# Kernel tuning notes

Hardware: AMD Instinct MI355X
Metric: run time of the kernel (lower is better)

Reference implementation:

```python
import jax, jax.numpy as jnp
import numpy as np

B, N, IN_DIM = 2, 2048, 512
D_MODEL, N_HEADS, N_CLASSES = 1024, 16, 1024


def sin_pos_encoding(n, d):
    # Matches SinPositionalEncoding buffer pe[:n]
    pos = jnp.arange(n, dtype=jnp.float32)[:, None]
    div = jnp.exp(jnp.arange(0, d, 2, dtype=jnp.float32) * (-np.log(10000.0) / d))
    pe = jnp.zeros((n, d), dtype=jnp.float32)
    pe = pe.at[:, 0::2].set(jnp.sin(pos * div))
    pe = pe.at[:, 1::2].set(jnp.cos(pos * div))
    return pe


def setup_inputs() -> dict:
    key = jax.random.key(0)
    ks = jax.random.split(key, 9)
    s_emb = (2.0 / (IN_DIM + D_MODEL)) ** 0.5
    s_qk = (2.0 / (2 * D_MODEL)) ** 0.5
    s_v = (2.0 / (D_MODEL + 1)) ** 0.5
    s_o = (2.0 / (N_HEADS + D_MODEL)) ** 0.5
    s_dec = (2.0 / (D_MODEL + N_CLASSES)) ** 0.5
    return {
        'X': jax.random.normal(ks[0], (B, N, IN_DIM), dtype=jnp.float32),
        'emb_w': jax.random.normal(ks[1], (IN_DIM, D_MODEL), dtype=jnp.float32) * s_emb,
        'emb_b': jax.random.normal(ks[2], (D_MODEL,), dtype=jnp.float32) * 0.01,
        'Wq': jax.random.normal(ks[3], (N_HEADS, D_MODEL, D_MODEL), dtype=jnp.float32) * s_qk,
        'Wk': jax.random.normal(ks[4], (N_HEADS, D_MODEL, D_MODEL), dtype=jnp.float32) * s_qk,
        'Wv': jax.random.normal(ks[5], (N_HEADS, D_MODEL, 1), dtype=jnp.float32) * s_v,
        'Wo': jax.random.normal(ks[6], (N_HEADS, D_MODEL), dtype=jnp.float32) * s_o,
        'dec_w': jax.random.normal(ks[7], (D_MODEL, N_CLASSES), dtype=jnp.float32) * s_dec,
        'dec_b': jax.random.normal(ks[8], (N_CLASSES,), dtype=jnp.float32) * 0.01,
    }


def reference(X, emb_w, emb_b, Wq, Wk, Wv, Wo, dec_w, dec_b):
    b, n, _ = X.shape
    d = emb_w.shape[1]
    h = X @ emb_w + emb_b                       # [b, n, d]
    h = h + sin_pos_encoding(n, d)[None]        # positional encoding
    Q = jnp.einsum('bnd,hde->bhne', h, Wq)      # [b, H, n, d]
    K = jnp.einsum('bnd,hde->bhne', h, Wk)      # [b, H, n, d]
    V = jnp.einsum('bnd,hdv->bhnv', h, Wv)      # [b, H, n, 1]
    scores = jnp.einsum('bhqe,bhke->bhqk', Q, K) / jnp.sqrt(jnp.float32(d))
    # mask[:, 0] = 1 is applied MULTIPLICATIVELY before softmax: column 0 -> 0
    scores = scores.at[..., 0].set(0.0)
    attn = jax.nn.softmax(scores, axis=-1)      # [b, H, n, n]
    ctx = jnp.einsum('bhqk,bhkv->bhqv', attn, V)  # [b, H, n, 1]
    ctx = jnp.transpose(ctx, (0, 2, 1, 3)).reshape(b, n, -1)  # [b, n, H]
    out = ctx @ Wo                              # [b, n, d]
    out = out @ dec_w + dec_b                   # [b, n, n_classes]
    return out
```

## Files before the change

kernel.cpp:

```cpp
#include <hip/hip_runtime.h>
#include <cstdint>

typedef __attribute__((ext_vector_type(8))) short bf16x8;
typedef __attribute__((ext_vector_type(4))) float f32x4;

#define B_ 2
#define N_ 2048
#define IN_DIM_ 512
#define D_ 1024
#define H_ 16

__device__ __forceinline__ unsigned short f2bf(float f) {
  uint32_t u = __float_as_uint(f);
  u = u + 0x7fffu + ((u >> 16) & 1u);
  return (unsigned short)(u >> 16);
}
__device__ __forceinline__ float bf2f(unsigned short b) {
  return __uint_as_float(((uint32_t)b) << 16);
}

__device__ __forceinline__ void gll16(const void* g, void* l) {
  __builtin_amdgcn_global_load_lds(
      (const __attribute__((address_space(1))) uint32_t*)g,
      (__attribute__((address_space(3))) uint32_t*)l, 16, 0, 0);
}

__global__ __launch_bounds__(256) void cast_bf16(const float* __restrict__ X,
                                                 unsigned short* __restrict__ O, int n) {
  int i = (blockIdx.x * 256 + threadIdx.x) * 4;
  if (i + 3 < n) {
    f32x4 v = *(const f32x4*)(X + i);
    uint32_t p0 = (uint32_t)f2bf(v[0]) | ((uint32_t)f2bf(v[1]) << 16);
    uint32_t p1 = (uint32_t)f2bf(v[2]) | ((uint32_t)f2bf(v[3]) << 16);
    *(uint32_t*)(O + i) = p0;
    *(uint32_t*)(O + i + 2) = p1;
  }
}

__global__ __launch_bounds__(256) void transpose_cast(const float* __restrict__ W,
                                                      unsigned short* __restrict__ WT,
                                                      int K, int N) {
  __shared__ float t[32][33];
  const int tx = threadIdx.x, ty = threadIdx.y;
  const int x = blockIdx.x * 32 + tx;
  const int y = blockIdx.y * 32 + ty;
  #pragma unroll
  for (int i = 0; i < 4; ++i)
    t[ty + i * 8][tx] = W[(size_t)(y + i * 8) * N + x];
  __syncthreads();
  const int ox = blockIdx.y * 32 + tx;
  #pragma unroll
  for (int i = 0; i < 4; ++i) {
    const int oy = blockIdx.x * 32 + ty + i * 8;
    WT[(size_t)oy * K + ox] = f2bf(t[tx][ty + i * 8]);
  }
}

__global__ __launch_bounds__(256) void gemm_embed(
    const unsigned short* __restrict__ Xbf, const unsigned short* __restrict__ EbT,
    const float* __restrict__ emb_b, unsigned short* __restrict__ Hbf) {
  const int tid = threadIdx.x, l = tid & 63, w = tid >> 6;
  const int wm = w >> 1, wn = w & 1;
  const int bm = blockIdx.y * 128, bn = blockIdx.x * 128;
  __shared__ unsigned short As[128 * 32], Bs[128 * 32];
  const unsigned short* Ab = Xbf + (size_t)bm * IN_DIM_;
  const unsigned short* Bb = EbT + (size_t)bn * IN_DIM_;
  f32x4 acc[4][4] = {};
  const int lr = l >> 2, lc = (l & 3) * 8;
  for (int k0 = 0; k0 < IN_DIM_; k0 += 32) {
    #pragma unroll
    for (int i = 0; i < 2; ++i) {
      const int c = w * 2 + i;
      gll16(Ab + (size_t)(c * 16 + lr) * IN_DIM_ + k0 + lc, As + c * 512);
      gll16(Bb + (size_t)(c * 16 + lr) * IN_DIM_ + k0 + lc, Bs + c * 512);
    }
    __syncthreads();
    bf16x8 af[4], bfr[4];
    #pragma unroll
    for (int f = 0; f < 4; ++f) {
      af[f]  = *(const bf16x8*)(As + (wm * 64 + f * 16 + (l & 15)) * 32 + (l >> 4) * 8);
      bfr[f] = *(const bf16x8*)(Bs + (wn * 64 + f * 16 + (l & 15)) * 32 + (l >> 4) * 8);
    }
    #pragma unroll
    for (int fr = 0; fr < 4; ++fr)
      #pragma unroll
      for (int fc = 0; fc < 4; ++fc)
        acc[fr][fc] = __builtin_amdgcn_mfma_f32_16x16x32_bf16(af[fr], bfr[fc], acc[fr][fc], 0, 0, 0);
    __syncthreads();
  }
  const float kF = -0.017988946039015983f;
  #pragma unroll
  for (int fr = 0; fr < 4; ++fr) {
    #pragma unroll
    for (int fc = 0; fc < 4; ++fc) {
      const int col = bn + wn * 64 + fc * 16 + (l & 15);
      const float eb = emb_b[col];
      const float fac = expf((float)(col >> 1) * kF);
      #pragma unroll
      for (int j = 0; j < 4; ++j) {
        const int row = bm + wm * 64 + fr * 16 + (l >> 4) * 4 + j;
        const float pos = (float)(row & (N_ - 1));
        const float ang = pos * fac;
        const float pe = (col & 1) ? cosf(ang) : sinf(ang);
        float v = acc[fr][fc][j] + eb + pe;
        float o = __shfl_xor(v, 1);
        unsigned short mb = f2bf(v), ob = f2bf(o);
        uint32_t pk = (l & 1) ? ((uint32_t)ob | ((uint32_t)mb << 16))
                              : ((uint32_t)mb | ((uint32_t)ob << 16));
        const bool mine = (l & 1) ? (j >= 2) : (j < 2);
        if (mine)
          *(uint32_t*)(Hbf + (size_t)row * D_ + (col & ~1)) = pk;
      }
    }
  }
}

__global__ __launch_bounds__(256) void gemm_nt(
    const unsigned short* __restrict__ A, const unsigned short* __restrict__ Bm,
    unsigned short* __restrict__ O, int K, long aZ, long bZ, long oZ, int swz) {
  int bx = blockIdx.x, by = blockIdx.y, bz = blockIdx.z;
  if (swz) {
    const int nx = gridDim.x, ny = gridDim.y;
    const int nwg = nx * ny * gridDim.z;
    const int bid = bx + nx * (by + ny * bz);
    const int wid = (bid & 7) * (nwg >> 3) + (bid >> 3);
    bx = wid % nx;
    const int rest = wid / nx;
    by = rest % ny;
    bz = rest / ny;
  }
  const int z = bz;
  const int tid = threadIdx.x, l = tid & 63, w = tid >> 6;
  const int wm = w >> 1, wn = w & 1;
  const int bm = by * 128, bn = bx * 128;
  const int ldo = gridDim.x * 128;
  __shared__ unsigned short As[128 * 32], Bs[128 * 32];
  const unsigned short* Ab = A + (size_t)z * aZ + (size_t)bm * K;
  const unsigned short* Bb = Bm + (size_t)z * bZ + (size_t)bn * K;
  f32x4 acc[4][4] = {};
  const int lr = l >> 2, lc = (l & 3) * 8;
  for (int k0 = 0; k0 < K; k0 += 32) {
    #pragma unroll
    for (int i = 0; i < 2; ++i) {
      const int c = w * 2 + i;
      gll16(Ab + (size_t)(c * 16 + lr) * K + k0 + lc, As + c * 512);
      gll16(Bb + (size_t)(c * 16 + lr) * K + k0 + lc, Bs + c * 512);
    }
    __syncthreads();
    bf16x8 af[4], bfr[4];
    #pragma unroll
    for (int f = 0; f < 4; ++f) {
      af[f]  = *(const bf16x8*)(As + (wm * 64 + f * 16 + (l & 15)) * 32 + (l >> 4) * 8);
      bfr[f] = *(const bf16x8*)(Bs + (wn * 64 + f * 16 + (l & 15)) * 32 + (l >> 4) * 8);
    }
    #pragma unroll
    for (int fr = 0; fr < 4; ++fr)
      #pragma unroll
      for (int fc = 0; fc < 4; ++fc)
        acc[fr][fc] = __builtin_amdgcn_mfma_f32_16x16x32_bf16(af[fr], bfr[fc], acc[fr][fc], 0, 0, 0);
    __syncthreads();
  }
  unsigned short* obase = O + (size_t)z * oZ;
  #pragma unroll
  for (int fr = 0; fr < 4; ++fr) {
    #pragma unroll
    for (int fc = 0; fc < 4; ++fc) {
      const int col = bn + wn * 64 + fc * 16 + (l & 15);
      #pragma unroll
      for (int j = 0; j < 4; ++j) {
        const int row = bm + wm * 64 + fr * 16 + (l >> 4) * 4 + j;
        float v = acc[fr][fc][j];
        float o = __shfl_xor(v, 1);
        unsigned short mb = f2bf(v), ob = f2bf(o);
        uint32_t pk = (l & 1) ? ((uint32_t)ob | ((uint32_t)mb << 16))
                              : ((uint32_t)mb | ((uint32_t)ob << 16));
        const bool mine = (l & 1) ? (j >= 2) : (j < 2);
        if (mine)
          *(uint32_t*)(obase + (size_t)row * ldo + (col & ~1)) = pk;
      }
    }
  }
}

__global__ __launch_bounds__(256) void v_kernel(
    const unsigned short* __restrict__ Hbf, const float* __restrict__ Wv,
    float* __restrict__ V) {
  const int l = threadIdx.x & 63, w = threadIdx.x >> 6;
  const int ng = blockIdx.x * 4 + w;
  const int b = ng >> 11, n = ng & (N_ - 1);
  const unsigned short* hr = Hbf + (size_t)ng * D_;
  float hv[16];
  #pragma unroll
  for (int i = 0; i < 2; ++i) {
    bf16x8 x = *(const bf16x8*)(hr + l * 16 + i * 8);
    #pragma unroll
    for (int j = 0; j < 8; ++j) hv[i * 8 + j] = bf2f((unsigned short)x[j]);
  }
  for (int h = 0; h < H_; ++h) {
    const float* wr = Wv + (size_t)h * D_ + l * 16;
    float s = 0.f;
    #pragma unroll
    for (int i = 0; i < 4; ++i) {
      f32x4 w4 = *(const f32x4*)(wr + i * 4);
      s += hv[i*4+0]*w4[0] + hv[i*4+1]*w4[1] + hv[i*4+2]*w4[2] + hv[i*4+3]*w4[3];
    }
    #pragma unroll
    for (int m = 1; m < 64; m <<= 1) s += __shfl_xor(s, m);
    if (l == 0) V[((size_t)b * H_ + h) * N_ + n] = s;
  }
}

__global__ __launch_bounds__(256) void score_flash(
    const unsigned short* __restrict__ G, const unsigned short* __restrict__ Hb,
    const float* __restrict__ V, float* __restrict__ Pp) {
  const int bid = blockIdx.x;
  const int wid = (bid & 7) * 512 + (bid >> 3);
  const int kt = wid & 15, qt = (wid >> 4) & 15, h = wid >> 8;
  const int tid = threadIdx.x, l = tid & 63, w = tid >> 6;
  const int wm = w >> 1, wn = w & 1;
  __shared__ unsigned short As[2 * 128 * 32], Bs[2 * 128 * 32];
  __shared__ float sb[2][128][2];
  const unsigned short* Ab = G + ((size_t)h * N_ + qt * 128) * D_;
  const unsigned short* Bb = Hb + (size_t)(kt * 128) * D_;
  const float* Vf = V + (size_t)h * N_;
  f32x4 acc[4][4] = {};
  const int lr = l >> 2, lc = (l & 3) * 8;
  for (int k0 = 0; k0 < D_; k0 += 64) {
    #pragma unroll
    for (int half = 0; half < 2; ++half) {
      #pragma unroll
      for (int i = 0; i < 2; ++i) {
        const int c = w * 2 + i;
        gll16(Ab + (size_t)(c * 16 + lr) * D_ + k0 + half * 32 + lc,
              As + half * 4096 + c * 512);
        gll16(Bb + (size_t)(c * 16 + lr) * D_ + k0 + half * 32 + lc,
              Bs + half * 4096 + c * 512);
      }
    }
    __syncthreads();
    #pragma unroll
    for (int half = 0; half < 2; ++half) {
      bf16x8 af[4], bfr[4];
      #pragma unroll
      for (int f = 0; f < 4; ++f) {
        af[f]  = *(const bf16x8*)(As + half * 4096 + (wm * 64 + f * 16 + (l & 15)) * 32 + (l >> 4) * 8);
        bfr[f] = *(const bf16x8*)(Bs + half * 4096 + (wn * 64 + f * 16 + (l & 15)) * 32 + (l >> 4) * 8);
      }
      #pragma unroll
      for (int fr = 0; fr < 4; ++fr)
        #pragma unroll
        for (int fc = 0; fc < 4; ++fc)
          acc[fr][fc] = __builtin_amdgcn_mfma_f32_16x16x32_bf16(af[fr], bfr[fc], acc[fr][fc], 0, 0, 0);
    }
    __syncthreads();
  }
  float vv[4];
  #pragma unroll
  for (int fc = 0; fc < 4; ++fc)
    vv[fc] = Vf[kt * 128 + wn * 64 + fc * 16 + (l & 15)];
  #pragma unroll
  for (int fr = 0; fr < 4; ++fr) {
    #pragma unroll
    for (int j = 0; j < 4; ++j) {
      float s4[4];
      #pragma unroll
      for (int fc = 0; fc < 4; ++fc) s4[fc] = acc[fr][fc][j] * 0.03125f;
      if (kt == 0 && wn == 0 && (l & 15) == 0) s4[0] = 0.0f;
      float ps = 0.f, pv = 0.f;
      #pragma unroll
      for (int fc = 0; fc < 4; ++fc) {
        const float e = __expf(s4[fc] - 8.0f);
        ps += e; pv += e * vv[fc];
      }
      ps += __shfl_xor(ps, 1); pv += __shfl_xor(pv, 1);
      ps += __shfl_xor(ps, 2); pv += __shfl_xor(pv, 2);
      ps += __shfl_xor(ps, 4); pv += __shfl_xor(pv, 4);
      ps += __shfl_xor(ps, 8); pv += __shfl_xor(pv, 8);
      if ((l & 15) == 0) {
        const int r = wm * 64 + fr * 16 + (l >> 4) * 4 + j;
        sb[wn][r][0] = ps; sb[wn][r][1] = pv;
      }
    }
  }
  __syncthreads();
  if (tid < 128) {
    const int r = tid;
    float* p = Pp + (((size_t)h * 16 + kt) * N_ + qt * 128 + r) * 2;
    p[0] = sb[0][r][0] + sb[1][r][0];
    p[1] = sb[0][r][1] + sb[1][r][1];
  }
}

__global__ __launch_bounds__(256) void merge16(const float* __restrict__ Pp,
                                               float* __restrict__ ctx) {
  const int idx = blockIdx.x * 256 + threadIdx.x;
  const int h = idx >> 11, q = idx & (N_ - 1);
  float L = 0.f, O = 0.f;
  #pragma unroll
  for (int kt = 0; kt < 16; ++kt) {
    const float* p = Pp + (((size_t)h * 16 + kt) * N_ + q) * 2;
    L += p[0]; O += p[1];
  }
  ctx[(size_t)q * H_ + h] = O / L;
}

__global__ __launch_bounds__(256) void wodec_kernel(
    const float* __restrict__ Wo, const float* __restrict__ dec_w, float* __restrict__ M) {
  const int idx = blockIdx.x * 256 + threadIdx.x;
  const int h = idx >> 10, c = idx & 1023;
  float s = 0.f;
  #pragma unroll 4
  for (int d = 0; d < D_; ++d) s += Wo[h * D_ + d] * dec_w[(size_t)d * 1024 + c];
  M[idx] = s;
}

__global__ __launch_bounds__(256) void final_kernel(
    const float* __restrict__ ctx, const float* __restrict__ M,
    const float* __restrict__ dec_b, float* __restrict__ out) {
  const int idx = blockIdx.x * 256 + threadIdx.x;
  const int c = idx & 1023;
  const float* cr = ctx + (size_t)(idx >> 10) * H_;
  float s = dec_b[c];
  #pragma unroll
  for (int h = 0; h < H_; ++h) s += cr[h] * M[h * 1024 + c];
  out[idx] = s;
}

extern "C" void kernel_launch(void* const* d_in, const int* in_sizes, int n_in,
                              void* d_out, int out_size, void* d_ws, size_t ws_size,
                              hipStream_t stream) {
  const float* X     = (const float*)d_in[0];
  const float* emb_w = (const float*)d_in[1];
  const float* emb_b = (const float*)d_in[2];
  const float* Wq    = (const float*)d_in[3];
  const float* Wk    = (const float*)d_in[4];
  const float* Wv    = (const float*)d_in[5];
  const float* Wo    = (const float*)d_in[6];
  const float* dec_b = (const float*)d_in[8];
  const float* dec_w = (const float*)d_in[7];
  float* out = (float*)d_out;
  (void)in_sizes; (void)n_in; (void)out_size;

  char* ws = (char*)d_ws;
  unsigned short* Hbf = (unsigned short*)(ws);
  unsigned short* Wkq = (unsigned short*)(ws + ((size_t)8 << 20));
  float* Vb  = (float*)(ws + ((size_t)40 << 20));
  float* ctx = (float*)(ws + ((size_t)40 << 20) + ((size_t)256 << 10));
  float* Mw  = (float*)(ws + ((size_t)40 << 20) + ((size_t)512 << 10));
  char* S = ws + ((size_t)41 << 20);
  unsigned short* Xbf  = (unsigned short*)(S);
  unsigned short* EbT  = (unsigned short*)(S + ((size_t)4 << 20));
  unsigned short* Wqbf = (unsigned short*)(S);
  unsigned short* Wkbf = (unsigned short*)(S + ((size_t)32 << 20));
  unsigned short* G    = (unsigned short*)(S);
  float* Pp = (float*)d_out;

  const size_t need = ((size_t)41 << 20) + ((size_t)64 << 20);
  if (ws_size < need) return;

  cast_bf16<<<2048, 256, 0, stream>>>(X, Xbf, B_ * N_ * IN_DIM_);
  transpose_cast<<<dim3(32, 16, 1), dim3(32, 8), 0, stream>>>(emb_w, EbT, IN_DIM_, D_);
  gemm_embed<<<dim3(8, 32), 256, 0, stream>>>(Xbf, EbT, emb_b, Hbf);
  cast_bf16<<<16384, 256, 0, stream>>>(Wq, Wqbf, H_ * D_ * D_);
  cast_bf16<<<16384, 256, 0, stream>>>(Wk, Wkbf, H_ * D_ * D_);
  gemm_nt<<<dim3(8, 8, 16), 256, 0, stream>>>(Wkbf, Wqbf, Wkq, D_,
                                              (long)D_ * D_, (long)D_ * D_, (long)D_ * D_, 1);
  v_kernel<<<1024, 256, 0, stream>>>(Hbf, Wv, Vb);
  wodec_kernel<<<64, 256, 0, stream>>>(Wo, dec_w, Mw);

  for (int b = 0; b < B_; ++b) {
    const unsigned short* Hb = Hbf + (size_t)b * N_ * D_;
    gemm_nt<<<dim3(8, 16, 16), 256, 0, stream>>>(Hb, Wkq, G, D_,
                                                 0L, (long)D_ * D_, (long)N_ * D_, 1);
    score_flash<<<4096, 256, 0, stream>>>(G, Hb, Vb + (size_t)b * H_ * N_, Pp);
    merge16<<<128, 256, 0, stream>>>(Pp, ctx + (size_t)b * N_ * H_);
  }
  final_kernel<<<16384, 256, 0, stream>>>(ctx, Mw, dec_b, out);
}
```

Before: 874.1 us.

## Merge Wq/Wk casts and V/Wo-dec kernels, deepen gemm_nt K step

Replaces the two separate Wq and Wk bf16 cast launches with one combined launch, and folds the Wo·dec_w product into the V projection kernel as extra blocks. gemm_nt now loads two 32-wide K slices per barrier pair, processing 64 K per iteration. The goal is fewer kernel launches and fewer barriers per K step. The cost is doubled LDS use in gemm_nt, which may lower occupancy.

```diff
diff --git a/kernel.cpp b/kernel.cpp
--- a/kernel.cpp
+++ b/kernel.cpp
@@ -35,6 +35,22 @@
     *(uint32_t*)(O + i) = p0;
     *(uint32_t*)(O + i + 2) = p1;
   }
+}
+
+__global__ __launch_bounds__(256) void cast_bf16x2(const float* __restrict__ X0,
+                                                   const float* __restrict__ X1,
+                                                   unsigned short* __restrict__ O0,
+                                                   unsigned short* __restrict__ O1, int n) {
+  int i = (blockIdx.x * 256 + threadIdx.x) * 4;
+  const bool second = (i >= n);
+  const int j = second ? i - n : i;
+  const float* X = second ? X1 : X0;
+  unsigned short* O = second ? O1 : O0;
+  f32x4 v = *(const f32x4*)(X + j);
+  uint32_t p0 = (uint32_t)f2bf(v[0]) | ((uint32_t)f2bf(v[1]) << 16);
+  uint32_t p1 = (uint32_t)f2bf(v[2]) | ((uint32_t)f2bf(v[3]) << 16);
+  *(uint32_t*)(O + j) = p0;
+  *(uint32_t*)(O + j + 2) = p1;
 }
 
 __global__ __launch_bounds__(256) void transpose_cast(const float* __restrict__ W,
@@ -134,30 +150,38 @@
   const int wm = w >> 1, wn = w & 1;
   const int bm = by * 128, bn = bx * 128;
   const int ldo = gridDim.x * 128;
-  __shared__ unsigned short As[128 * 32], Bs[128 * 32];
+  __shared__ unsigned short As[2 * 128 * 32], Bs[2 * 128 * 32];
   const unsigned short* Ab = A + (size_t)z * aZ + (size_t)bm * K;
   const unsigned short* Bb = Bm + (size_t)z * bZ + (size_t)bn * K;
   f32x4 acc[4][4] = {};
   const int lr = l >> 2, lc = (l & 3) * 8;
-  for (int k0 = 0; k0 < K; k0 += 32) {
-    #pragma unroll
-    for (int i = 0; i < 2; ++i) {
-      const int c = w * 2 + i;
-      gll16(Ab + (size_t)(c * 16 + lr) * K + k0 + lc, As + c * 512);
-      gll16(Bb + (size_t)(c * 16 + lr) * K + k0 + lc, Bs + c * 512);
-    }
-    __syncthreads();
-    bf16x8 af[4], bfr[4];
-    #pragma unroll
-    for (int f = 0; f < 4; ++f) {
-      af[f]  = *(const bf16x8*)(As + (wm * 64 + f * 16 + (l & 15)) * 32 + (l >> 4) * 8);
-      bfr[f] = *(const bf16x8*)(Bs + (wn * 64 + f * 16 + (l & 15)) * 32 + (l >> 4) * 8);
-    }
-    #pragma unroll
-    for (int fr = 0; fr < 4; ++fr)
-      #pragma unroll
-      for (int fc = 0; fc < 4; ++fc)
-        acc[fr][fc] = __builtin_amdgcn_mfma_f32_16x16x32_bf16(af[fr], bfr[fc], acc[fr][fc], 0, 0, 0);
+  for (int k0 = 0; k0 < K; k0 += 64) {
+    #pragma unroll
+    for (int half = 0; half < 2; ++half) {
+      #pragma unroll
+      for (int i = 0; i < 2; ++i) {
+        const int c = w * 2 + i;
+        gll16(Ab + (size_t)(c * 16 + lr) * K + k0 + half * 32 + lc,
+              As + half * 4096 + c * 512);
+        gll16(Bb + (size_t)(c * 16 + lr) * K + k0 + half * 32 + lc,
+              Bs + half * 4096 + c * 512);
+      }
+    }
+    __syncthreads();
+    #pragma unroll
+    for (int half = 0; half < 2; ++half) {
+      bf16x8 af[4], bfr[4];
+      #pragma unroll
+      for (int f = 0; f < 4; ++f) {
+        af[f]  = *(const bf16x8*)(As + half * 4096 + (wm * 64 + f * 16 + (l & 15)) * 32 + (l >> 4) * 8);
+        bfr[f] = *(const bf16x8*)(Bs + half * 4096 + (wn * 64 + f * 16 + (l & 15)) * 32 + (l >> 4) * 8);
+      }
+      #pragma unroll
+      for (int fr = 0; fr < 4; ++fr)
+        #pragma unroll
+        for (int fc = 0; fc < 4; ++fc)
+          acc[fr][fc] = __builtin_amdgcn_mfma_f32_16x16x32_bf16(af[fr], bfr[fc], acc[fr][fc], 0, 0, 0);
+    }
     __syncthreads();
   }
   unsigned short* obase = O + (size_t)z * oZ;
@@ -182,31 +206,41 @@
   }
 }
 
-__global__ __launch_bounds__(256) void v_kernel(
+__global__ __launch_bounds__(256) void v_wodec_kernel(
     const unsigned short* __restrict__ Hbf, const float* __restrict__ Wv,
-    float* __restrict__ V) {
-  const int l = threadIdx.x & 63, w = threadIdx.x >> 6;
-  const int ng = blockIdx.x * 4 + w;
-  const int b = ng >> 11, n = ng & (N_ - 1);
-  const unsigned short* hr = Hbf + (size_t)ng * D_;
-  float hv[16];
-  #pragma unroll
-  for (int i = 0; i < 2; ++i) {
-    bf16x8 x = *(const bf16x8*)(hr + l * 16 + i * 8);
-    #pragma unroll
-    for (int j = 0; j < 8; ++j) hv[i * 8 + j] = bf2f((unsigned short)x[j]);
-  }
-  for (int h = 0; h < H_; ++h) {
-    const float* wr = Wv + (size_t)h * D_ + l * 16;
+    float* __restrict__ V, const float* __restrict__ Wo,
+    const float* __restrict__ dec_w, float* __restrict__ M) {
+  if (blockIdx.x < 1024) {
+    const int l = threadIdx.x & 63, w = threadIdx.x >> 6;
+    const int ng = blockIdx.x * 4 + w;
+    const int b = ng >> 11, n = ng & (N_ - 1);
+    const unsigned short* hr = Hbf + (size_t)ng * D_;
+    float hv[16];
+    #pragma unroll
+    for (int i = 0; i < 2; ++i) {
+      bf16x8 x = *(const bf16x8*)(hr + l * 16 + i * 8);
+      #pragma unroll
+      for (int j = 0; j < 8; ++j) hv[i * 8 + j] = bf2f((unsigned short)x[j]);
+    }
+    for (int h = 0; h < H_; ++h) {
+      const float* wr = Wv + (size_t)h * D_ + l * 16;
+      float s = 0.f;
+      #pragma unroll
+      for (int i = 0; i < 4; ++i) {
+        f32x4 w4 = *(const f32x4*)(wr + i * 4);
+        s += hv[i*4+0]*w4[0] + hv[i*4+1]*w4[1] + hv[i*4+2]*w4[2] + hv[i*4+3]*w4[3];
+      }
+      #pragma unroll
+      for (int m = 1; m < 64; m <<= 1) s += __shfl_xor(s, m);
+      if (l == 0) V[((size_t)b * H_ + h) * N_ + n] = s;
+    }
+  } else {
+    const int idx = (blockIdx.x - 1024) * 256 + threadIdx.x;
+    const int h = idx >> 10, c = idx & 1023;
     float s = 0.f;
-    #pragma unroll
-    for (int i = 0; i < 4; ++i) {
-      f32x4 w4 = *(const f32x4*)(wr + i * 4);
-      s += hv[i*4+0]*w4[0] + hv[i*4+1]*w4[1] + hv[i*4+2]*w4[2] + hv[i*4+3]*w4[3];
-    }
-    #pragma unroll
-    for (int m = 1; m < 64; m <<= 1) s += __shfl_xor(s, m);
-    if (l == 0) V[((size_t)b * H_ + h) * N_ + n] = s;
+    #pragma unroll 4
+    for (int d = 0; d < D_; ++d) s += Wo[h * D_ + d] * dec_w[(size_t)d * 1024 + c];
+    M[idx] = s;
   }
 }
 
@@ -304,16 +338,6 @@
   ctx[(size_t)q * H_ + h] = O / L;
 }
 
-__global__ __launch_bounds__(256) void wodec_kernel(
-    const float* __restrict__ Wo, const float* __restrict__ dec_w, float* __restrict__ M) {
-  const int idx = blockIdx.x * 256 + threadIdx.x;
-  const int h = idx >> 10, c = idx & 1023;
-  float s = 0.f;
-  #pragma unroll 4
-  for (int d = 0; d < D_; ++d) s += Wo[h * D_ + d] * dec_w[(size_t)d * 1024 + c];
-  M[idx] = s;
-}
-
 __global__ __launch_bounds__(256) void final_kernel(
     const float* __restrict__ ctx, const float* __restrict__ M,
     const float* __restrict__ dec_b, float* __restrict__ out) {
@@ -361,12 +385,10 @@
   cast_bf16<<<2048, 256, 0, stream>>>(X, Xbf, B_ * N_ * IN_DIM_);
   transpose_cast<<<dim3(32, 16, 1), dim3(32, 8), 0, stream>>>(emb_w, EbT, IN_DIM_, D_);
   gemm_embed<<<dim3(8, 32), 256, 0, stream>>>(Xbf, EbT, emb_b, Hbf);
-  cast_bf16<<<16384, 256, 0, stream>>>(Wq, Wqbf, H_ * D_ * D_);
-  cast_bf16<<<16384, 256, 0, stream>>>(Wk, Wkbf, H_ * D_ * D_);
+  cast_bf16x2<<<32768, 256, 0, stream>>>(Wq, Wk, Wqbf, Wkbf, H_ * D_ * D_);
   gemm_nt<<<dim3(8, 8, 16), 256, 0, stream>>>(Wkbf, Wqbf, Wkq, D_,
                                               (long)D_ * D_, (long)D_ * D_, (long)D_ * D_, 1);
-  v_kernel<<<1024, 256, 0, stream>>>(Hbf, Wv, Vb);
-  wodec_kernel<<<64, 256, 0, stream>>>(Wo, dec_w, Mw);
+  v_wodec_kernel<<<1088, 256, 0, stream>>>(Hbf, Wv, Vb, Wo, dec_w, Mw);
 
   for (int b = 0; b < B_; ++b) {
     const unsigned short* Hb = Hbf + (size_t)b * N_ * D_;
```

Result: faster. 843.4 us (-3.5%).
